# Kernel optimization log

Measured on AMD Instinct MI355X. Metric: run time of the kernel, lower is better.

The kernel has to match this reference:

```python
import jax, jax.numpy as jnp
import numpy as np

GRID_H, GRID_W, INPUT_DIM = 256, 256, 64
BATCH = 4096


def setup_inputs() -> dict:
    key = jax.random.key(0)
    k_in, k_w = jax.random.split(key)
    inputs = jax.random.uniform(k_in, (BATCH, INPUT_DIM), dtype=jnp.float32)
    # SOM weights initialized uniform[0,1) as in the original layer
    weights_map = jax.random.uniform(k_w, (GRID_H, GRID_W, INPUT_DIM), dtype=jnp.float32)
    return {"inputs": inputs, "weights_map": weights_map}


def reference(inputs, weights_map):
    """Inference forward of SOM2dLayer: find BMU coords + quantization error.

    inputs:      [B, D]
    weights_map: [H, W, D]
    returns (bmu_indices [B,2] int32, quantization_errors [B] float32)
    """
    H, W, D = weights_map.shape
    flat_w = weights_map.reshape(H * W, D)            # [N, D]
    x2 = jnp.sum(inputs * inputs, axis=1, keepdims=True)      # [B, 1]
    w2 = jnp.sum(flat_w * flat_w, axis=1)                     # [N]
    d2 = x2 - 2.0 * (inputs @ flat_w.T) + w2                  # [B, N]
    d2 = jnp.maximum(d2, 0.0)                                 # numerical floor
    bmu_flat = jnp.argmin(d2, axis=1)                         # [B]
    bmu_y = (bmu_flat // W).astype(jnp.int32)
    bmu_x = (bmu_flat % W).astype(jnp.int32)
    bmu_indices = jnp.stack([bmu_y, bmu_x], axis=1)           # [B, 2]
    min_d2 = jnp.take_along_axis(d2, bmu_flat[:, None], axis=1)[:, 0]
    quantization_errors = jnp.sqrt(min_d2)                    # [B]
    return bmu_indices, quantization_errors
```

## Files before the change

### kernel.cpp

```cpp
#include <hip/hip_runtime.h>
#include <math.h>


typedef short  bf16x8 __attribute__((ext_vector_type(8)));
typedef float  f32x4  __attribute__((ext_vector_type(4)));
typedef unsigned short u16;
typedef unsigned short u16x4 __attribute__((ext_vector_type(4)));

constexpr int D    = 64;
constexpr int NW   = 65536;
constexpr int B    = 4096;
constexpr int NSUB = 256;
constexpr int NFINE = NW / 16;
constexpr float MARG_HALF = 0.15f;

constexpr int STRIPS   = 16;
constexpr int STRIP_N  = NW / STRIPS;
constexpr int ROWS_BLK = 128;

__device__ inline u16 bf16u(float f) {
    union { float f; unsigned u; } v; v.f = f;
    unsigned b = v.u;
    b += 0x7fffu + ((b >> 16) & 1u);
    return (u16)(b >> 16);
}

__device__ inline u16 bf16up(float f) {
    union { float f; unsigned u; } v; v.f = f;
    unsigned h = v.u >> 16;
    if ((v.u & 0xFFFFu) && !(v.u >> 31)) h += 1;
    return (u16)h;
}

__device__ __forceinline__ void gload_lds16(const void* g, void* l) {
    __builtin_amdgcn_global_load_lds(
        (const __attribute__((address_space(1))) unsigned int*)g,
        (__attribute__((address_space(3))) unsigned int*)l, 16, 0, 0);
}

__global__ __launch_bounds__(256) void k_wprep(const float* __restrict__ w,
                                               u16* __restrict__ whi,
                                               float* __restrict__ w2c) {
    int n = blockIdx.x * 256 + threadIdx.x;
    const float4* wr = reinterpret_cast<const float4*>(w + (size_t)n * D);
    u16* orow = whi + (size_t)n * D;
    float a0 = 0.f, a1 = 0.f, a2 = 0.f, a3 = 0.f;
#pragma unroll
    for (int h = 0; h < 8; ++h) {
        float4 v0 = wr[2 * h], v1 = wr[2 * h + 1];
        a0 = fmaf(v0.x, v0.x, a0); a1 = fmaf(v0.y, v0.y, a1);
        a2 = fmaf(v0.z, v0.z, a2); a3 = fmaf(v0.w, v0.w, a3);
        a0 = fmaf(v1.x, v1.x, a0); a1 = fmaf(v1.y, v1.y, a1);
        a2 = fmaf(v1.z, v1.z, a2); a3 = fmaf(v1.w, v1.w, a3);
        bf16x8 o = {(short)bf16u(v0.x), (short)bf16u(v0.y),
                    (short)bf16u(v0.z), (short)bf16u(v0.w),
                    (short)bf16u(v1.x), (short)bf16u(v1.y),
                    (short)bf16u(v1.z), (short)bf16u(v1.w)};
        *reinterpret_cast<bf16x8*>(orow + 8 * h) = o;
    }
    w2c[n] = -0.5f * ((a0 + a1) + (a2 + a3));
}

__global__ __launch_bounds__(256) void k_xprep(const float* __restrict__ x,
                                               u16* __restrict__ xhi) {
    int r = blockIdx.x * 256 + threadIdx.x;
    const float4* xr = reinterpret_cast<const float4*>(x + (size_t)r * D);
    u16* orow = xhi + (size_t)r * D;
#pragma unroll
    for (int h = 0; h < 8; ++h) {
        float4 v0 = xr[2 * h], v1 = xr[2 * h + 1];
        bf16x8 o = {(short)bf16u(v0.x), (short)bf16u(v0.y),
                    (short)bf16u(v0.z), (short)bf16u(v0.w),
                    (short)bf16u(v1.x), (short)bf16u(v1.y),
                    (short)bf16u(v1.z), (short)bf16u(v1.w)};
        *reinterpret_cast<bf16x8*>(orow + 8 * h) = o;
    }
}

template <int WRITE_FINE>
__global__ __launch_bounds__(256, 2) void k_screen0(
        const u16* __restrict__ whi, const u16* __restrict__ xhi,
        const float* __restrict__ w2c, float* __restrict__ pm,
        u16* __restrict__ pmf) {
    __shared__ __align__(16) char smem[2][32768];
    const int bid   = blockIdx.x;
    const int strip = bid & 15;
    const int rbk   = bid >> 4;
    const int tid   = threadIdx.x;
    const int wv    = tid >> 6;
    const int lane  = tid & 63;
    const int col   = lane & 15;
    const int kg    = lane >> 4;
    const int row0  = rbk * ROWS_BLK;

    bf16x8 a[8][2];
#pragma unroll
    for (int rg = 0; rg < 8; ++rg)
#pragma unroll
        for (int h = 0; h < 2; ++h)
            a[rg][h] = *reinterpret_cast<const bf16x8*>(
                xhi + (size_t)(row0 + rg * 16 + col) * D + h * 32 + kg * 8);

    const char* wbase = (const char*)whi + (size_t)strip * STRIP_N * (D * 2);
    unsigned srcoff[8];
#pragma unroll
    for (int i = 0; i < 8; ++i) {
        unsigned o = (unsigned)(i * 256 + tid) * 16;
        srcoff[i] = o ^ (((o >> 7) & 7u) << 4);
    }

    const unsigned msk = (unsigned)(col & 7) << 4;
    const float* w2s = w2c + strip * STRIP_N;

    float mx[8][4];
#pragma unroll
    for (int rg = 0; rg < 8; ++rg)
#pragma unroll
        for (int r = 0; r < 4; ++r) mx[rg][r] = -3.4e38f;

    auto STAGE = [&](int bf, int panel) {
#pragma unroll
        for (int i = 0; i < 8; ++i)
            gload_lds16(wbase + (size_t)panel * 32768 + srcoff[i],
                        &smem[bf][i * 4096 + wv * 1024]);
    };

    STAGE(0, 0);
    __syncthreads();

    for (int p = 0; p < 16; ++p) {
        if (p < 15) STAGE((p + 1) & 1, p + 1);

        const char* buf = smem[p & 1];
        const float* w2p = w2s + p * 256;
#pragma unroll
        for (int t = 0; t < 4; ++t) {
            const int nloc = wv * 64 + t * 16 + col;
            const unsigned u0 = (unsigned)nloc * 128 + kg * 16;
            const bf16x8 b0 = *reinterpret_cast<const bf16x8*>(buf + (u0 ^ msk));
            const bf16x8 b1 = *reinterpret_cast<const bf16x8*>(buf + ((u0 + 64) ^ msk));
            const float c = w2p[nloc];
#pragma unroll
            for (int rg = 0; rg < 8; ++rg) {
                f32x4 acc = {c, c, c, c};
                acc = __builtin_amdgcn_mfma_f32_16x16x32_bf16(a[rg][0], b0, acc, 0, 0, 0);
                acc = __builtin_amdgcn_mfma_f32_16x16x32_bf16(a[rg][1], b1, acc, 0, 0, 0);
                mx[rg][0] = fmaxf(mx[rg][0], acc[0]);
                mx[rg][1] = fmaxf(mx[rg][1], acc[1]);
                mx[rg][2] = fmaxf(mx[rg][2], acc[2]);
                mx[rg][3] = fmaxf(mx[rg][3], acc[3]);
            }
        }

        if ((p & 3) == 3) {
            const int chunk = p >> 2;
            const int sub = strip * 16 + chunk * 4 + wv;

            if (WRITE_FINE) {
                const int f = sub * 16 + col;
#pragma unroll
                for (int rg = 0; rg < 8; ++rg) {
                    u16x4 h = {bf16up(mx[rg][0]), bf16up(mx[rg][1]),
                               bf16up(mx[rg][2]), bf16up(mx[rg][3])};
                    *reinterpret_cast<u16x4*>(
                        pmf + (size_t)f * B + row0 + rg * 16 + kg * 4) = h;
                }
            }

#pragma unroll
            for (int rg = 0; rg < 8; ++rg) {
                float v0 = mx[rg][0], v1 = mx[rg][1], v2 = mx[rg][2], v3 = mx[rg][3];
#pragma unroll
                for (int s = 1; s < 16; s <<= 1) {
                    v0 = fmaxf(v0, __shfl_xor(v0, s, 64));
                    v1 = fmaxf(v1, __shfl_xor(v1, s, 64));
                    v2 = fmaxf(v2, __shfl_xor(v2, s, 64));
                    v3 = fmaxf(v3, __shfl_xor(v3, s, 64));
                }
                float vv = v0;
                vv = (col == 1) ? v1 : vv;
                vv = (col == 2) ? v2 : vv;
                vv = (col == 3) ? v3 : vv;
                if (col < 4)
                    pm[(size_t)(row0 + rg * 16 + kg * 4 + col) * NSUB + sub] = vv;
                mx[rg][0] = -3.4e38f; mx[rg][1] = -3.4e38f;
                mx[rg][2] = -3.4e38f; mx[rg][3] = -3.4e38f;
            }
        }
        __syncthreads();
    }
}

template <int FINE>
__global__ __launch_bounds__(256) void k_rescore(
        const float* __restrict__ x, const float* __restrict__ w,
        const float* __restrict__ w2c, const float* __restrict__ pm,
        const u16* __restrict__ pmf, float* __restrict__ out) {
    const int wv   = threadIdx.x >> 6;
    const int lane = threadIdx.x & 63;
    const int row  = blockIdx.x * 4 + wv;

    float pv[4];
#pragma unroll
    for (int it = 0; it < 4; ++it)
        pv[it] = pm[(size_t)row * NSUB + it * 64 + lane];
    float gm = fmaxf(fmaxf(pv[0], pv[1]), fmaxf(pv[2], pv[3]));
#pragma unroll
    for (int s = 1; s < 64; s <<= 1) gm = fmaxf(gm, __shfl_xor(gm, s, 64));
    const float thr = gm - MARG_HALF;

    const float4* xr = reinterpret_cast<const float4*>(x + (size_t)row * D);
    float4 xq[16];
#pragma unroll
    for (int q = 0; q < 16; ++q) xq[q] = xr[q];

    float bestv = 3.4e38f;
    int   besti = 0x7fffffff;

#pragma unroll
    for (int it = 0; it < 4; ++it) {
        unsigned long long bm = __ballot(pv[it] >= thr);
        while (bm) {
            int sb = __ffsll(bm) - 1;
            bm &= bm - 1;
            int sub = it * 64 + sb;
            int strip = sub >> 4, chunk = (sub >> 2) & 3, wvv = sub & 3;
            int base0 = strip * 4096 + chunk * 1024 + wvv * 64;

            if (FINE) {
                float fv = -3.4e38f;
                if (lane < 16) {
                    union { unsigned u; float f; } c;
                    c.u = (unsigned)pmf[(size_t)(sub * 16 + lane) * B + row] << 16;
                    fv = c.f;
                }
                unsigned long long fm = __ballot(fv >= thr);
                while (fm) {
                    int colq = __ffsll(fm) - 1;
                    fm &= fm - 1;
                    int j = lane & 15, q = lane >> 4;
                    int n = base0 + (j >> 2) * 256 + (j & 3) * 16 + colq;
                    const float4* wr = reinterpret_cast<const float4*>(w + (size_t)n * D);
                    float d0 = 0.f, d1 = 0.f, d2 = 0.f, d3 = 0.f;
#pragma unroll
                    for (int k = 0; k < 4; ++k) {
                        float4 wq = wr[q * 4 + k];
                        float4 xv = xq[q * 4 + k];
                        d0 = fmaf(xv.x, wq.x, d0); d1 = fmaf(xv.y, wq.y, d1);
                        d2 = fmaf(xv.z, wq.z, d2); d3 = fmaf(xv.w, wq.w, d3);
                    }
                    float d = (d0 + d1) + (d2 + d3);
                    d += __shfl_xor(d, 16, 64);
                    d += __shfl_xor(d, 32, 64);
                    float val = -2.f * (d + w2c[n]);
                    if (val < bestv || (val == bestv && n < besti)) { bestv = val; besti = n; }
                }
            } else {
                int nb = base0 + lane;
#pragma unroll
                for (int q4 = 0; q4 < 4; ++q4) {
                    int n = nb + q4 * 256;
                    const float4* wr = reinterpret_cast<const float4*>(w + (size_t)n * D);
                    float d0 = 0.f, d1 = 0.f, d2 = 0.f, d3 = 0.f;
#pragma unroll
                    for (int q = 0; q < 16; ++q) {
                        float4 wq = wr[q];
                        d0 = fmaf(xq[q].x, wq.x, d0);
                        d1 = fmaf(xq[q].y, wq.y, d1);
                        d2 = fmaf(xq[q].z, wq.z, d2);
                        d3 = fmaf(xq[q].w, wq.w, d3);
                    }
                    float dot = (d0 + d1) + (d2 + d3);
                    float val = -2.f * (dot + w2c[n]);
                    if (val < bestv || (val == bestv && n < besti)) { bestv = val; besti = n; }
                }
            }
        }
    }
#pragma unroll
    for (int s = 1; s < 64; s <<= 1) {
        float ov = __shfl_xor(bestv, s, 64);
        int   oi = __shfl_xor(besti, s, 64);
        if (ov < bestv || (ov == bestv && oi < besti)) { bestv = ov; besti = oi; }
    }
    if (lane == 0) {
        float a0 = 0.f, a1 = 0.f, a2 = 0.f, a3 = 0.f;
#pragma unroll
        for (int q = 0; q < 16; ++q) {
            a0 = fmaf(xq[q].x, xq[q].x, a0);
            a1 = fmaf(xq[q].y, xq[q].y, a1);
            a2 = fmaf(xq[q].z, xq[q].z, a2);
            a3 = fmaf(xq[q].w, xq[q].w, a3);
        }
        float x2 = (a0 + a1) + (a2 + a3);
        float d2f = x2 + bestv;
        if (d2f < 0.f) d2f = 0.f;
        out[row * 2 + 0] = (float)(besti >> 8);
        out[row * 2 + 1] = (float)(besti & 255);
        out[2 * B + row] = sqrtf(d2f);
    }
}

__global__ __launch_bounds__(256) void fb_w2(const float* __restrict__ w,
                                             float* __restrict__ w2) {
    int n = blockIdx.x * 256 + threadIdx.x;
    const float4* wr = reinterpret_cast<const float4*>(w + (size_t)n * D);
    float a0 = 0.f, a1 = 0.f, a2 = 0.f, a3 = 0.f;
#pragma unroll
    for (int q = 0; q < 16; ++q) {
        float4 v = wr[q];
        a0 = fmaf(v.x, v.x, a0); a1 = fmaf(v.y, v.y, a1);
        a2 = fmaf(v.z, v.z, a2); a3 = fmaf(v.w, v.w, a3);
    }
    w2[n] = (a0 + a1) + (a2 + a3);
}

__global__ __launch_bounds__(256) void fb_main(const float* __restrict__ x,
                                               const float* __restrict__ w,
                                               const float* __restrict__ w2,
                                               float* __restrict__ ps,
                                               int* __restrict__ pi) {
    constexpr int NSTRIP = NW / 32;
    const int rb    = blockIdx.x & 15;
    const int strip = blockIdx.x >> 4;
    const int row   = rb * 256 + threadIdx.x;
    float xr[D];
    const float4* xrow = reinterpret_cast<const float4*>(x + (size_t)row * D);
#pragma unroll
    for (int q = 0; q < 16; ++q) {
        float4 v = xrow[q];
        xr[q * 4 + 0] = v.x; xr[q * 4 + 1] = v.y;
        xr[q * 4 + 2] = v.z; xr[q * 4 + 3] = v.w;
    }
    float best = 3.4e38f; int bidx = 0;
    const int n0 = strip * NSTRIP, n1 = n0 + NSTRIP;
    for (int n = n0; n < n1; ++n) {
        const float* wr = w + (size_t)n * D;
        float a0 = 0.f, a1 = 0.f, a2 = 0.f, a3 = 0.f;
#pragma unroll
        for (int d = 0; d < D; d += 4) {
            a0 = fmaf(xr[d + 0], wr[d + 0], a0);
            a1 = fmaf(xr[d + 1], wr[d + 1], a1);
            a2 = fmaf(xr[d + 2], wr[d + 2], a2);
            a3 = fmaf(xr[d + 3], wr[d + 3], a3);
        }
        float s = fmaf(-2.f, (a0 + a1) + (a2 + a3), w2[n]);
        if (s < best) { best = s; bidx = n; }
    }
    ps[(size_t)strip * B + row] = best;
    pi[(size_t)strip * B + row] = bidx;
}

__global__ __launch_bounds__(256) void fb_merge(const float* __restrict__ x,
                                                const float* __restrict__ ps,
                                                const int* __restrict__ pi,
                                                float* __restrict__ out) {
    int row = blockIdx.x * 256 + threadIdx.x;
    float bs = 3.5e38f; int bi = 0;
    for (int t = 0; t < 32; ++t) {
        float s = ps[(size_t)t * B + row];
        int   i = pi[(size_t)t * B + row];
        if (s < bs || (s == bs && i < bi)) { bs = s; bi = i; }
    }
    const float4* xrow = reinterpret_cast<const float4*>(x + (size_t)row * D);
    float a0 = 0.f, a1 = 0.f, a2 = 0.f, a3 = 0.f;
#pragma unroll
    for (int q = 0; q < 16; ++q) {
        float4 v = xrow[q];
        a0 = fmaf(v.x, v.x, a0); a1 = fmaf(v.y, v.y, a1);
        a2 = fmaf(v.z, v.z, a2); a3 = fmaf(v.w, v.w, a3);
    }
    float x2 = (a0 + a1) + (a2 + a3);
    float d2 = x2 + bs;
    if (d2 < 0.f) d2 = 0.f;
    out[row * 2 + 0] = (float)(bi >> 8);
    out[row * 2 + 1] = (float)(bi & 255);
    out[2 * B + row] = sqrtf(d2);
}

extern "C" void kernel_launch(void* const* d_in, const int* in_sizes, int n_in,
                              void* d_out, int out_size, void* d_ws, size_t ws_size,
                              hipStream_t stream) {
    const float* x = (const float*)d_in[0];
    const float* w = (const float*)d_in[1];
    float* out = (float*)d_out;

    const size_t whi_sz = (size_t)NW * D * 2;
    const size_t xhi_sz = (size_t)B * D * 2;
    const size_t w2c_sz = (size_t)NW * 4;
    const size_t pm_sz  = (size_t)B * NSUB * 4;
    const size_t pmf_sz = (size_t)NFINE * B * 2;
    const size_t need_c = whi_sz + xhi_sz + w2c_sz + pm_sz;
    const size_t need_f = need_c + pmf_sz;

    if (ws_size >= need_c) {
        char* p = (char*)d_ws;
        u16*   whi = (u16*)p;   p += whi_sz;
        u16*   xhi = (u16*)p;   p += xhi_sz;
        float* w2c = (float*)p; p += w2c_sz;
        float* pm  = (float*)p; p += pm_sz;
        u16*   pmf = (u16*)p;

        k_wprep<<<NW / 256, 256, 0, stream>>>(w, whi, w2c);
        k_xprep<<<B / 256, 256, 0, stream>>>(x, xhi);
        if (ws_size >= need_f) {
            k_screen0<1><<<STRIPS * (B / ROWS_BLK), 256, 0, stream>>>(whi, xhi, w2c, pm, pmf);
            k_rescore<1><<<B / 4, 256, 0, stream>>>(x, w, w2c, pm, pmf, out);
        } else {
            k_screen0<0><<<STRIPS * (B / ROWS_BLK), 256, 0, stream>>>(whi, xhi, w2c, pm, pmf);
            k_rescore<0><<<B / 4, 256, 0, stream>>>(x, w, w2c, pm, pmf, out);
        }
    } else {
        float* w2 = (float*)d_ws;
        float* ps = w2 + NW;
        int*   pi = (int*)(ps + (size_t)32 * B);
        fb_w2<<<NW / 256, 256, 0, stream>>>(w, w2);
        fb_main<<<16 * 32, 256, 0, stream>>>(x, w, w2, ps, pi);
        fb_merge<<<B / 256, 256, 0, stream>>>(x, ps, pi, out);
    }
}
```

Baseline: 115.6 us.

## Give each wave a private triple-buffered LDS pipeline and drop block barriers in screening

```diff
diff --git a/kernel.cpp b/kernel.cpp
--- a/kernel.cpp
+++ b/kernel.cpp
@@ -7,16 +7,18 @@
 typedef unsigned short u16;
 typedef unsigned short u16x4 __attribute__((ext_vector_type(4)));
 
-constexpr int D    = 64;
-constexpr int NW   = 65536;
-constexpr int B    = 4096;
-constexpr int NSUB = 256;
+constexpr int D     = 64;
+constexpr int NW    = 65536;
+constexpr int B     = 4096;
+constexpr int NSUB  = 256;
 constexpr int NFINE = NW / 16;
 constexpr float MARG_HALF = 0.15f;
 
-constexpr int STRIPS   = 16;
+constexpr int STRIPS   = 32;
 constexpr int STRIP_N  = NW / STRIPS;
 constexpr int ROWS_BLK = 128;
+constexpr int WAVE_N   = STRIP_N / 4;
+constexpr int NMICRO   = WAVE_N / 32;
 
 __device__ inline u16 bf16u(float f) {
     union { float f; unsigned u; } v; v.f = f;
@@ -38,60 +40,61 @@
         (__attribute__((address_space(3))) unsigned int*)l, 16, 0, 0);
 }
 
-__global__ __launch_bounds__(256) void k_wprep(const float* __restrict__ w,
-                                               u16* __restrict__ whi,
-                                               float* __restrict__ w2c) {
-    int n = blockIdx.x * 256 + threadIdx.x;
-    const float4* wr = reinterpret_cast<const float4*>(w + (size_t)n * D);
-    u16* orow = whi + (size_t)n * D;
-    float a0 = 0.f, a1 = 0.f, a2 = 0.f, a3 = 0.f;
-#pragma unroll
-    for (int h = 0; h < 8; ++h) {
-        float4 v0 = wr[2 * h], v1 = wr[2 * h + 1];
-        a0 = fmaf(v0.x, v0.x, a0); a1 = fmaf(v0.y, v0.y, a1);
-        a2 = fmaf(v0.z, v0.z, a2); a3 = fmaf(v0.w, v0.w, a3);
-        a0 = fmaf(v1.x, v1.x, a0); a1 = fmaf(v1.y, v1.y, a1);
-        a2 = fmaf(v1.z, v1.z, a2); a3 = fmaf(v1.w, v1.w, a3);
-        bf16x8 o = {(short)bf16u(v0.x), (short)bf16u(v0.y),
-                    (short)bf16u(v0.z), (short)bf16u(v0.w),
-                    (short)bf16u(v1.x), (short)bf16u(v1.y),
-                    (short)bf16u(v1.z), (short)bf16u(v1.w)};
-        *reinterpret_cast<bf16x8*>(orow + 8 * h) = o;
-    }
-    w2c[n] = -0.5f * ((a0 + a1) + (a2 + a3));
-}
-
-__global__ __launch_bounds__(256) void k_xprep(const float* __restrict__ x,
-                                               u16* __restrict__ xhi) {
-    int r = blockIdx.x * 256 + threadIdx.x;
-    const float4* xr = reinterpret_cast<const float4*>(x + (size_t)r * D);
-    u16* orow = xhi + (size_t)r * D;
-#pragma unroll
-    for (int h = 0; h < 8; ++h) {
-        float4 v0 = xr[2 * h], v1 = xr[2 * h + 1];
-        bf16x8 o = {(short)bf16u(v0.x), (short)bf16u(v0.y),
-                    (short)bf16u(v0.z), (short)bf16u(v0.w),
-                    (short)bf16u(v1.x), (short)bf16u(v1.y),
-                    (short)bf16u(v1.z), (short)bf16u(v1.w)};
-        *reinterpret_cast<bf16x8*>(orow + 8 * h) = o;
+__global__ __launch_bounds__(256) void k_prep(const float* __restrict__ w,
+                                              const float* __restrict__ x,
+                                              u16* __restrict__ whi,
+                                              u16* __restrict__ xhi,
+                                              float* __restrict__ w2c) {
+    const int idx = blockIdx.x * 256 + threadIdx.x;
+    if (idx < NW) {
+        const float4* wr = reinterpret_cast<const float4*>(w + (size_t)idx * D);
+        u16* orow = whi + (size_t)idx * D;
+        float a0 = 0.f, a1 = 0.f, a2 = 0.f, a3 = 0.f;
+#pragma unroll
+        for (int h = 0; h < 8; ++h) {
+            float4 v0 = wr[2 * h], v1 = wr[2 * h + 1];
+            a0 = fmaf(v0.x, v0.x, a0); a1 = fmaf(v0.y, v0.y, a1);
+            a2 = fmaf(v0.z, v0.z, a2); a3 = fmaf(v0.w, v0.w, a3);
+            a0 = fmaf(v1.x, v1.x, a0); a1 = fmaf(v1.y, v1.y, a1);
+            a2 = fmaf(v1.z, v1.z, a2); a3 = fmaf(v1.w, v1.w, a3);
+            bf16x8 o = {(short)bf16u(v0.x), (short)bf16u(v0.y),
+                        (short)bf16u(v0.z), (short)bf16u(v0.w),
+                        (short)bf16u(v1.x), (short)bf16u(v1.y),
+                        (short)bf16u(v1.z), (short)bf16u(v1.w)};
+            *reinterpret_cast<bf16x8*>(orow + 8 * h) = o;
+        }
+        w2c[idx] = -0.5f * ((a0 + a1) + (a2 + a3));
+    } else {
+        const int r = idx - NW;
+        const float4* xr = reinterpret_cast<const float4*>(x + (size_t)r * D);
+        u16* orow = xhi + (size_t)r * D;
+#pragma unroll
+        for (int h = 0; h < 8; ++h) {
+            float4 v0 = xr[2 * h], v1 = xr[2 * h + 1];
+            bf16x8 o = {(short)bf16u(v0.x), (short)bf16u(v0.y),
+                        (short)bf16u(v0.z), (short)bf16u(v0.w),
+                        (short)bf16u(v1.x), (short)bf16u(v1.y),
+                        (short)bf16u(v1.z), (short)bf16u(v1.w)};
+            *reinterpret_cast<bf16x8*>(orow + 8 * h) = o;
+        }
     }
 }
 
 template <int WRITE_FINE>
-__global__ __launch_bounds__(256, 2) void k_screen0(
+__global__ __launch_bounds__(256, 3) void k_screen0(
         const u16* __restrict__ whi, const u16* __restrict__ xhi,
         const float* __restrict__ w2c, float* __restrict__ pm,
         u16* __restrict__ pmf) {
-    __shared__ __align__(16) char smem[2][32768];
+    __shared__ __align__(16) char smem[4][3][4096];
     const int bid   = blockIdx.x;
-    const int strip = bid & 15;
-    const int rbk   = bid >> 4;
-    const int tid   = threadIdx.x;
-    const int wv    = tid >> 6;
-    const int lane  = tid & 63;
+    const int strip = bid & 31;
+    const int rbk   = bid >> 5;
+    const int wv    = threadIdx.x >> 6;
+    const int lane  = threadIdx.x & 63;
     const int col   = lane & 15;
     const int kg    = lane >> 4;
     const int row0  = rbk * ROWS_BLK;
+    const int W0    = strip * STRIP_N + wv * WAVE_N;
 
     bf16x8 a[8][2];
 #pragma unroll
@@ -101,45 +104,47 @@
             a[rg][h] = *reinterpret_cast<const bf16x8*>(
                 xhi + (size_t)(row0 + rg * 16 + col) * D + h * 32 + kg * 8);
 
-    const char* wbase = (const char*)whi + (size_t)strip * STRIP_N * (D * 2);
-    unsigned srcoff[8];
-#pragma unroll
-    for (int i = 0; i < 8; ++i) {
-        unsigned o = (unsigned)(i * 256 + tid) * 16;
-        srcoff[i] = o ^ (((o >> 7) & 7u) << 4);
-    }
+    const char* wsrc = (const char*)whi + (size_t)W0 * 128;
+    unsigned soff[4];
+#pragma unroll
+    for (int i = 0; i < 4; ++i) {
+        unsigned o = (unsigned)(i * 64 + lane) * 16;
+        soff[i] = o ^ (((o >> 7) & 7u) << 4);
+    }
+    char* lds0 = &smem[wv][0][0];
+
+    auto STAGE = [&](int m) {
+        const char* gsl = wsrc + (size_t)m * 4096;
+        char* dst = lds0 + (m % 3) * 4096;
+#pragma unroll
+        for (int i = 0; i < 4; ++i)
+            gload_lds16(gsl + soff[i], dst + i * 1024);
+    };
+
+    STAGE(0);
+    STAGE(1);
 
     const unsigned msk = (unsigned)(col & 7) << 4;
-    const float* w2s = w2c + strip * STRIP_N;
-
     float mx[8][4];
 #pragma unroll
     for (int rg = 0; rg < 8; ++rg)
 #pragma unroll
         for (int r = 0; r < 4; ++r) mx[rg][r] = -3.4e38f;
 
-    auto STAGE = [&](int bf, int panel) {
-#pragma unroll
-        for (int i = 0; i < 8; ++i)
-            gload_lds16(wbase + (size_t)panel * 32768 + srcoff[i],
-                        &smem[bf][i * 4096 + wv * 1024]);
-    };
-
-    STAGE(0, 0);
-    __syncthreads();
-
-    for (int p = 0; p < 16; ++p) {
-        if (p < 15) STAGE((p + 1) & 1, p + 1);
-
-        const char* buf = smem[p & 1];
-        const float* w2p = w2s + p * 256;
-#pragma unroll
-        for (int t = 0; t < 4; ++t) {
-            const int nloc = wv * 64 + t * 16 + col;
-            const unsigned u0 = (unsigned)nloc * 128 + kg * 16;
-            const bf16x8 b0 = *reinterpret_cast<const bf16x8*>(buf + (u0 ^ msk));
-            const bf16x8 b1 = *reinterpret_cast<const bf16x8*>(buf + ((u0 + 64) ^ msk));
-            const float c = w2p[nloc];
+    for (int m = 0; m < NMICRO; ++m) {
+        if (m + 2 < NMICRO) STAGE(m + 2);
+        if (m + 2 < NMICRO)      asm volatile("s_waitcnt vmcnt(8)" ::: "memory");
+        else if (m + 1 < NMICRO) asm volatile("s_waitcnt vmcnt(4)" ::: "memory");
+        else                     asm volatile("s_waitcnt vmcnt(0)" ::: "memory");
+
+        const char* buf = lds0 + (m % 3) * 4096;
+#pragma unroll
+        for (int t = 0; t < 2; ++t) {
+            const int nl = t * 16 + col;
+            const unsigned g = (unsigned)nl * 128 + kg * 16;
+            const bf16x8 b0 = *reinterpret_cast<const bf16x8*>(buf + (g ^ msk));
+            const bf16x8 b1 = *reinterpret_cast<const bf16x8*>(buf + ((g + 64) ^ msk));
+            const float c = w2c[W0 + m * 32 + nl];
 #pragma unroll
             for (int rg = 0; rg < 8; ++rg) {
                 f32x4 acc = {c, c, c, c};
@@ -152,12 +157,11 @@
             }
         }
 
-        if ((p & 3) == 3) {
-            const int chunk = p >> 2;
-            const int sub = strip * 16 + chunk * 4 + wv;
+        if ((m & 7) == 7) {
+            const int s = strip * 8 + wv * 2 + (m >> 3);
 
             if (WRITE_FINE) {
-                const int f = sub * 16 + col;
+                const int f = s * 16 + col;
 #pragma unroll
                 for (int rg = 0; rg < 8; ++rg) {
                     u16x4 h = {bf16up(mx[rg][0]), bf16up(mx[rg][1]),
@@ -171,23 +175,22 @@
             for (int rg = 0; rg < 8; ++rg) {
                 float v0 = mx[rg][0], v1 = mx[rg][1], v2 = mx[rg][2], v3 = mx[rg][3];
 #pragma unroll
-                for (int s = 1; s < 16; s <<= 1) {
-                    v0 = fmaxf(v0, __shfl_xor(v0, s, 64));
-                    v1 = fmaxf(v1, __shfl_xor(v1, s, 64));
-                    v2 = fmaxf(v2, __shfl_xor(v2, s, 64));
-                    v3 = fmaxf(v3, __shfl_xor(v3, s, 64));
+                for (int sh = 1; sh < 16; sh <<= 1) {
+                    v0 = fmaxf(v0, __shfl_xor(v0, sh, 64));
+                    v1 = fmaxf(v1, __shfl_xor(v1, sh, 64));
+                    v2 = fmaxf(v2, __shfl_xor(v2, sh, 64));
+                    v3 = fmaxf(v3, __shfl_xor(v3, sh, 64));
                 }
                 float vv = v0;
                 vv = (col == 1) ? v1 : vv;
                 vv = (col == 2) ? v2 : vv;
                 vv = (col == 3) ? v3 : vv;
                 if (col < 4)
-                    pm[(size_t)(row0 + rg * 16 + kg * 4 + col) * NSUB + sub] = vv;
+                    pm[(size_t)(row0 + rg * 16 + kg * 4 + col) * NSUB + s] = vv;
                 mx[rg][0] = -3.4e38f; mx[rg][1] = -3.4e38f;
                 mx[rg][2] = -3.4e38f; mx[rg][3] = -3.4e38f;
             }
         }
-        __syncthreads();
     }
 }
 
@@ -223,9 +226,8 @@
         while (bm) {
             int sb = __ffsll(bm) - 1;
             bm &= bm - 1;
-            int sub = it * 64 + sb;
-            int strip = sub >> 4, chunk = (sub >> 2) & 3, wvv = sub & 3;
-            int base0 = strip * 4096 + chunk * 1024 + wvv * 64;
+            int sub   = it * 64 + sb;
+            int base0 = sub * 256;
 
             if (FINE) {
                 float fv = -3.4e38f;
@@ -239,7 +241,7 @@
                     int colq = __ffsll(fm) - 1;
                     fm &= fm - 1;
                     int j = lane & 15, q = lane >> 4;
-                    int n = base0 + (j >> 2) * 256 + (j & 3) * 16 + colq;
+                    int n = base0 + colq + 16 * j;
                     const float4* wr = reinterpret_cast<const float4*>(w + (size_t)n * D);
                     float d0 = 0.f, d1 = 0.f, d2 = 0.f, d3 = 0.f;
 #pragma unroll
@@ -256,10 +258,9 @@
                     if (val < bestv || (val == bestv && n < besti)) { bestv = val; besti = n; }
                 }
             } else {
-                int nb = base0 + lane;
 #pragma unroll
                 for (int q4 = 0; q4 < 4; ++q4) {
-                    int n = nb + q4 * 256;
+                    int n = base0 + q4 * 64 + lane;
                     const float4* wr = reinterpret_cast<const float4*>(w + (size_t)n * D);
                     float d0 = 0.f, d1 = 0.f, d2 = 0.f, d3 = 0.f;
 #pragma unroll
@@ -401,8 +402,7 @@
         float* pm  = (float*)p; p += pm_sz;
         u16*   pmf = (u16*)p;
 
-        k_wprep<<<NW / 256, 256, 0, stream>>>(w, whi, w2c);
-        k_xprep<<<B / 256, 256, 0, stream>>>(x, xhi);
+        k_prep<<<(NW + B) / 256, 256, 0, stream>>>(w, x, whi, xhi, w2c);
         if (ws_size >= need_f) {
             k_screen0<1><<<STRIPS * (B / ROWS_BLK), 256, 0, stream>>>(whi, xhi, w2c, pm, pmf);
             k_rescore<1><<<B / 4, 256, 0, stream>>>(x, w, w2c, pm, pmf, out);
```

Measured after the change: 123.8 us. 7.0% more time.
